# Kernel optimization log

Hardware: AMD Instinct MI355X
Metric: run time of the kernel (lower is better)

## Reference

```python
import jax, jax.numpy as jnp
import numpy as np

K_POS, K_NEG = 3, 2
MIN_D = 9  # min_dist=8 bumped to next odd, as in _nms_topk
BN_EPS = 1e-5


def _conv(x, w, pad):
    return jax.lax.conv_general_dilated(
        x, w, (1, 1), [(pad, pad), (pad, pad)],
        dimension_numbers=('NCHW', 'OIHW', 'NCHW'))


def _bn(x, g, b, m, v):
    scale = g * jax.lax.rsqrt(v + BN_EPS)  # inference-mode BN
    return x * scale[None, :, None, None] + (b - m * scale)[None, :, None, None]


def _head(x, w1, g1, b1, m1, v1, w2, g2, b2, m2, v2, w3, b3, out_hw):
    h = jax.nn.relu(_bn(_conv(x, w1, 1), g1, b1, m1, v1))
    h = jax.nn.relu(_bn(_conv(h, w2, 1), g2, b2, m2, v2))
    logits = _conv(h, w3, 0) + b3[None, :, None, None]
    B = logits.shape[0]
    # F.interpolate(mode='bilinear', align_corners=False) == half-pixel bilinear resize
    logits = jax.image.resize(logits, (B, 1, out_hw, out_hw), method='bilinear')
    return logits


def _sample_one(smap, key):
    # smap: [H, W] sigmoid heatmap for one sample
    H, W = smap.shape
    # --- positive points: NMS-style peak top-k ---
    local_max = jax.lax.reduce_window(
        smap, -jnp.inf, jax.lax.max, (MIN_D, MIN_D), (1, 1), 'SAME')
    is_peak = (smap == local_max) & (smap > 0.1)
    masked = jnp.where(is_peak, smap, -jnp.inf).reshape(-1)
    vals, idx = jax.lax.top_k(masked, K_POS)
    valid = jnp.isfinite(vals)  # slots corresponding to real peaks
    xs = jnp.where(valid, (idx % W).astype(jnp.float32), 0.0)
    ys = jnp.where(valid, (idx // W).astype(jnp.float32), 0.0)
    pos_lab = jnp.where(valid, 1, -1).astype(jnp.int32)
    # fallback: no peak at all -> single argmax point in slot 0
    amax = jnp.argmax(smap)
    any_peak = valid[0]
    xs = xs.at[0].set(jnp.where(any_peak, xs[0], (amax % W).astype(jnp.float32)))
    ys = ys.at[0].set(jnp.where(any_peak, ys[0], (amax // W).astype(jnp.float32)))
    pos_lab = pos_lab.at[0].set(1)  # slot 0 is always a positive point
    pos = jnp.stack([xs, ys], axis=1)  # [K_POS, 2] (x, y)
    # --- negative points: uniform sample from low-response region ---
    low = (smap < 0.3).reshape(-1)
    low_fb = (smap < smap.max()).reshape(-1)
    mask = jnp.where(jnp.any(low), low, low_fb)
    n = mask.sum()
    # stable argsort puts masked-in (True) flat indices first, in index order
    order = jnp.argsort(jnp.logical_not(mask))
    u = jax.random.uniform(key, (K_NEG,))
    ridx = jnp.minimum((u * jnp.maximum(n, 1).astype(jnp.float32)).astype(jnp.int32),
                       jnp.maximum(n - 1, 0))
    sel = order[ridx]
    neg = jnp.stack([sel % W, sel // W], axis=1).astype(jnp.float32)
    neg = jnp.where(n > 0, neg, jnp.zeros_like(neg))
    neg_lab = jnp.zeros((K_NEG,), jnp.int32)
    coords = jnp.concatenate([pos, neg], axis=0)      # [K_POS+K_NEG, 2]
    labels = jnp.concatenate([pos_lab, neg_lab], axis=0)
    return coords, labels


def setup_inputs() -> dict:
    key = jax.random.key(0)
    ks = jax.random.split(key, 4)
    B, C, h, w = 32, 256, 64, 64
    HID = 64
    x = jax.random.normal(ks[0], (B, C, h, w), jnp.float32)
    w1 = jax.random.normal(ks[1], (HID, C, 3, 3), jnp.float32) * 0.03  # kaiming-ish
    w2 = jax.random.normal(ks[2], (HID, HID, 3, 3), jnp.float32) * 0.06
    w3 = jax.random.normal(ks[3], (1, HID, 1, 1), jnp.float32) * 0.17
    b3 = jnp.full((1,), -2.0, jnp.float32)
    ones = jnp.ones((HID,), jnp.float32)
    zeros = jnp.zeros((HID,), jnp.float32)
    return {
        'encoder_features': x,
        'w1': w1, 'g1': ones, 'b1': zeros, 'm1': zeros, 'v1': ones,
        'w2': w2, 'g2': ones, 'b2': zeros, 'm2': zeros, 'v2': ones,
        'w3': w3, 'b3': b3,
        'output_size': 256,
    }


def reference(encoder_features, w1, g1, b1, m1, v1, w2, g2, b2, m2, v2, w3, b3, output_size):
    logits = _head(encoder_features, w1, g1, b1, m1, v1, w2, g2, b2, m2, v2, w3, b3, output_size)
    heatmap = jax.nn.sigmoid(logits)  # [B, 1, H, W]
    B = heatmap.shape[0]
    keys = jax.random.split(jax.random.key(42), B)
    coords, labels = jax.vmap(_sample_one)(heatmap[:, 0], keys)
    point_coords = coords[:, None].astype(jnp.float32)  # [B, 1, K, 2]
    point_labels = labels[:, None].astype(jnp.int32)    # [B, 1, K]
    return heatmap, point_coords, point_labels, logits
```

## Files before the change

### kernel.cpp

```cpp
#include <hip/hip_runtime.h>
#include <stdint.h>
#include <math.h>

#define NEG_INF (-__builtin_inff())
#define IDX_SENT 0x7fffffff

__device__ __forceinline__ void threefry2x32(uint32_t k0, uint32_t k1,
                                             uint32_t x0, uint32_t x1,
                                             uint32_t* o0, uint32_t* o1) {
  const uint32_t ks2 = k0 ^ k1 ^ 0x1BD11BDAu;
  uint32_t ks[3] = {k0, k1, ks2};
  const int rot[2][4] = {{13, 15, 26, 6}, {17, 29, 16, 24}};
  x0 += ks[0];
  x1 += ks[1];
#pragma unroll
  for (int i = 0; i < 5; ++i) {
#pragma unroll
    for (int j = 0; j < 4; ++j) {
      const int r = rot[i & 1][j];
      x0 += x1;
      x1 = (x1 << r) | (x1 >> (32 - r));
      x1 ^= x0;
    }
    x0 += ks[(i + 1) % 3];
    x1 += ks[(i + 2) % 3] + (uint32_t)(i + 1);
  }
  *o0 = x0;
  *o1 = x1;
}

__device__ __forceinline__ float bits_to_uniform(uint32_t bits) {
  return __uint_as_float((bits >> 9) | 0x3f800000u) - 1.0f;
}

__device__ __forceinline__ void top3_insert(float v, int idx, float tv[3], int ti[3]) {
  if ((v > tv[2]) || (v == tv[2] && idx < ti[2])) {
    tv[2] = v; ti[2] = idx;
    if ((tv[2] > tv[1]) || (tv[2] == tv[1] && ti[2] < ti[1])) {
      float fv = tv[1]; int fi = ti[1];
      tv[1] = tv[2]; ti[1] = ti[2];
      tv[2] = fv;     ti[2] = fi;
      if ((tv[1] > tv[0]) || (tv[1] == tv[0] && ti[1] < ti[0])) {
        fv = tv[0]; fi = ti[0];
        tv[0] = tv[1]; ti[0] = ti[1];
        tv[1] = fv;    ti[1] = fi;
      }
    }
  }
}

__global__ __launch_bounds__(256) void transpose_w4(
    const float* __restrict__ w, float* __restrict__ wt, int IC9) {
  const int idx = blockIdx.x * 256 + threadIdx.x;
  const int qrow = idx >> 6;
  const int oc = idx & 63;
  const float4 v = *(const float4*)&w[(size_t)oc * IC9 + qrow * 4];
  wt[(size_t)(qrow * 4 + 0) * 64 + oc] = v.x;
  wt[(size_t)(qrow * 4 + 1) * 64 + oc] = v.y;
  wt[(size_t)(qrow * 4 + 2) * 64 + oc] = v.z;
  wt[(size_t)(qrow * 4 + 3) * 64 + oc] = v.w;
}

template <int IC>
__global__ __launch_bounds__(256, 2) void conv3x3_bn_relu(
    const float* __restrict__ x, const float* __restrict__ wt,
    const float* __restrict__ g, const float* __restrict__ bb,
    const float* __restrict__ m, const float* __restrict__ vv,
    float* __restrict__ out) {
  __shared__ float xs[2][8][10][36];

  const int tid = threadIdx.x;
  const int blk = blockIdx.x;
  const int b = blk >> 4;
  const int tile = blk & 15;
  const int by = (tile >> 1) << 3;
  const int bx = (tile & 1) << 5;
  const int wv = __builtin_amdgcn_readfirstlane(tid >> 6);
  const int lane = tid & 63;
  const int r = lane & 7;
  const int lc = (lane >> 3) << 2;
  const int ocbase = wv << 4;

  const int sic = tid >> 5;
  const int sc = tid & 31;
  const int gx = bx + sc - 1;
  const bool cok = (gx >= 0) && (gx < 64);
  const bool xtra = (sc < 2);
  const int gx2 = bx + 31 + sc;
  const bool cok2 = xtra && (gx2 < 64);

  float acc[4][16];
#pragma unroll
  for (int p = 0; p < 4; ++p)
#pragma unroll
    for (int o = 0; o < 16; ++o) acc[p][o] = 0.0f;

  float pre[10];
  float preX[10];
  {
    const float* xp = x + ((size_t)b * IC + sic) * 4096;
#pragma unroll
    for (int rr = 0; rr < 10; ++rr) {
      const int gy = by + rr - 1;
      const bool rok = (gy >= 0) && (gy < 64);
      pre[rr] = 0.0f;
      preX[rr] = 0.0f;
      if (cok && rok) pre[rr] = xp[gy * 64 + gx];
      if (cok2 && rok) preX[rr] = xp[gy * 64 + gx2];
    }
#pragma unroll
    for (int rr = 0; rr < 10; ++rr) {
      xs[0][sic][rr][sc] = pre[rr];
      if (xtra) xs[0][sic][rr][32 + sc] = preX[rr];
    }
  }
  __syncthreads();

  int cur = 0;
  for (int icb = 0; icb < IC; icb += 8) {
    const bool has_next = (icb + 8) < IC;
    if (has_next) {
      const float* xp = x + ((size_t)b * IC + icb + 8 + sic) * 4096;
#pragma unroll
      for (int rr = 0; rr < 10; ++rr) {
        const int gy = by + rr - 1;
        const bool rok = (gy >= 0) && (gy < 64);
        pre[rr] = 0.0f;
        preX[rr] = 0.0f;
        if (cok && rok) pre[rr] = xp[gy * 64 + gx];
        if (cok2 && rok) preX[rr] = xp[gy * 64 + gx2];
      }
    }

    const float* wbase = wt + (size_t)icb * 9 * 64 + ocbase;
    for (int ic = 0; ic < 8; ++ic) {
#pragma unroll
      for (int ky = 0; ky < 3; ++ky) {
        float xv[6];
        *(float4*)&xv[0] = *(const float4*)&xs[cur][ic][r + ky][lc];
        *(float2*)&xv[4] = *(const float2*)&xs[cur][ic][r + ky][lc + 4];
#pragma unroll
        for (int kx = 0; kx < 3; ++kx) {
          const float4* wp4 = (const float4*)(wbase + (ic * 9 + ky * 3 + kx) * 64);
#pragma unroll
          for (int q = 0; q < 4; ++q) {
            const float4 w4 = wp4[q];
#pragma unroll
            for (int p = 0; p < 4; ++p) {
              acc[p][4 * q + 0] = fmaf(xv[kx + p], w4.x, acc[p][4 * q + 0]);
              acc[p][4 * q + 1] = fmaf(xv[kx + p], w4.y, acc[p][4 * q + 1]);
              acc[p][4 * q + 2] = fmaf(xv[kx + p], w4.z, acc[p][4 * q + 2]);
              acc[p][4 * q + 3] = fmaf(xv[kx + p], w4.w, acc[p][4 * q + 3]);
            }
          }
        }
      }
    }

    if (has_next) {
#pragma unroll
      for (int rr = 0; rr < 10; ++rr) {
        xs[cur ^ 1][sic][rr][sc] = pre[rr];
        if (xtra) xs[cur ^ 1][sic][rr][32 + sc] = preX[rr];
      }
    }
    __syncthreads();
    cur ^= 1;
  }

#pragma unroll
  for (int o = 0; o < 16; ++o) {
    const int oc = ocbase + o;
    const float sc2 = g[oc] * (1.0f / sqrtf(vv[oc] + 1e-5f));
    const float sh = bb[oc] - m[oc] * sc2;
    float4 v;
    v.x = fmaxf(fmaf(acc[0][o], sc2, sh), 0.0f);
    v.y = fmaxf(fmaf(acc[1][o], sc2, sh), 0.0f);
    v.z = fmaxf(fmaf(acc[2][o], sc2, sh), 0.0f);
    v.w = fmaxf(fmaf(acc[3][o], sc2, sh), 0.0f);
    *(float4*)&out[(((size_t)b * 64 + oc) * 64 + (by + r)) * 64 + bx + lc] = v;
  }
}

__global__ __launch_bounds__(256) void logits64_k(
    const float* __restrict__ h2, const float* __restrict__ w3,
    const float* __restrict__ b3, float* __restrict__ lg64) {
  const int blk = blockIdx.x;
  const int b = blk >> 4;
  const int p = ((blk & 15) << 8) + threadIdx.x;
  __shared__ float wvv[64];
  if (threadIdx.x < 64) wvv[threadIdx.x] = w3[threadIdx.x];
  __syncthreads();
  float s = b3[0];
  const float* hp = h2 + (size_t)b * 64 * 4096 + p;
  for (int oc = 0; oc < 64; ++oc)
    s = fmaf(hp[(size_t)oc * 4096], wvv[oc], s);
  lg64[b * 4096 + p] = s;
}

__global__ __launch_bounds__(256) void upsample_k(
    const float* __restrict__ lg64, float* __restrict__ logits,
    float* __restrict__ heat) {
  const int blk = blockIdx.x;
  const int b = blk >> 6;
  const int qq = ((blk & 63) << 10) + (threadIdx.x << 2);
  const float* lg = lg64 + b * 4096;
  const int oy = qq >> 8;
  const float sy = (float)oy * 0.25f - 0.375f;
  const float fy = floorf(sy);
  const int y0 = (int)fy;
  const float ty = sy - fy;
  const int y0c = y0 < 0 ? 0 : y0;
  const int y1c = (y0 + 1) > 63 ? 63 : (y0 + 1);
  const float* r0 = lg + y0c * 64;
  const float* r1 = lg + y1c * 64;
  float4 lo, he;
  float* lop = (float*)&lo;
  float* hep = (float*)&he;
#pragma unroll
  for (int j = 0; j < 4; ++j) {
    const int ox = (qq & 255) + j;
    const float sx = (float)ox * 0.25f - 0.375f;
    const float fx = floorf(sx);
    const int x0 = (int)fx;
    const float tx = sx - fx;
    const int x0c = x0 < 0 ? 0 : x0;
    const int x1c = (x0 + 1) > 63 ? 63 : (x0 + 1);
    const float v00 = r0[x0c], v01 = r0[x1c];
    const float v10 = r1[x0c], v11 = r1[x1c];
    const float vtop = v00 + (v01 - v00) * tx;
    const float vbot = v10 + (v11 - v10) * tx;
    const float val = vtop + (vbot - vtop) * ty;
    lop[j] = val;
    hep[j] = 1.0f / (1.0f + expf(-val));
  }
  const size_t o = (size_t)b * 65536 + qq;
  *(float4*)(logits + o) = lo;
  *(float4*)(heat + o) = he;
}

__global__ __launch_bounds__(256) void pos_stripe(
    const float* __restrict__ heat, float* __restrict__ cand) {
  const int b = blockIdx.x >> 4;
  const int stripe = blockIdx.x & 15;
  const int y0 = stripe << 4;
  const float* s = heat + (size_t)b * 65536;
  const int tid = threadIdx.x;
  __shared__ float sm[24][256];
  __shared__ float rm[24][256];
  __shared__ float rv[256 * 3];
  __shared__ int ri[256 * 3];
  __shared__ float mvv[256];
  __shared__ int mii[256];
  __shared__ float rv2[24];
  __shared__ int ri2[24];
  __shared__ float mv2[8];
  __shared__ int mi2[8];

  for (int l = tid; l < 24 * 256; l += 256) {
    const int rr = l >> 8, xx = l & 255;
    const int gy = y0 - 4 + rr;
    sm[rr][xx] = (gy >= 0 && gy < 256) ? s[gy * 256 + xx] : NEG_INF;
  }
  __syncthreads();
  for (int l = tid; l < 24 * 256; l += 256) {
    const int rr = l >> 8, xx = l & 255;
    const int lo = (xx - 4 < 0) ? 0 : xx - 4;
    const int hi = (xx + 4 > 255) ? 255 : xx + 4;
    float mx = NEG_INF;
    for (int x2 = lo; x2 <= hi; ++x2) mx = fmaxf(mx, sm[rr][x2]);
    rm[rr][xx] = mx;
  }
  __syncthreads();

  float tv[3] = {NEG_INF, NEG_INF, NEG_INF};
  int ti[3] = {IDX_SENT, IDX_SENT, IDX_SENT};
  float bmax = NEG_INF;
  int bidx = IDX_SENT;
  for (int l = tid; l < 16 * 256; l += 256) {
    const int ry = l >> 8, xx = l & 255;
    const int lr = ry + 4;
    const float v = sm[lr][xx];
    float lm = rm[lr - 4][xx];
#pragma unroll
    for (int d = -3; d <= 4; ++d) lm = fmaxf(lm, rm[lr + d][xx]);
    const int gidx = (y0 + ry) * 256 + xx;
    if (v > bmax) { bmax = v; bidx = gidx; }
    if (v == lm && v > 0.1f) top3_insert(v, gidx, tv, ti);
  }

  rv[tid * 3 + 0] = tv[0]; rv[tid * 3 + 1] = tv[1]; rv[tid * 3 + 2] = tv[2];
  ri[tid * 3 + 0] = ti[0]; ri[tid * 3 + 1] = ti[1]; ri[tid * 3 + 2] = ti[2];
  mvv[tid] = bmax; mii[tid] = bidx;
  __syncthreads();

  if (tid < 8) {
    float av[3] = {NEG_INF, NEG_INF, NEG_INF};
    int ai[3] = {IDX_SENT, IDX_SENT, IDX_SENT};
    float am = NEG_INF; int amI = IDX_SENT;
    for (int t = tid * 32; t < tid * 32 + 32; ++t) {
      for (int k = 0; k < 3; ++k) top3_insert(rv[t * 3 + k], ri[t * 3 + k], av, ai);
      if (mvv[t] > am || (mvv[t] == am && mii[t] < amI)) { am = mvv[t]; amI = mii[t]; }
    }
    rv2[tid * 3 + 0] = av[0]; rv2[tid * 3 + 1] = av[1]; rv2[tid * 3 + 2] = av[2];
    ri2[tid * 3 + 0] = ai[0]; ri2[tid * 3 + 1] = ai[1]; ri2[tid * 3 + 2] = ai[2];
    mv2[tid] = am; mi2[tid] = amI;
  }
  __syncthreads();

  if (tid == 0) {
    float fv[3] = {NEG_INF, NEG_INF, NEG_INF};
    int fi[3] = {IDX_SENT, IDX_SENT, IDX_SENT};
    for (int t = 0; t < 24; ++t) top3_insert(rv2[t], ri2[t], fv, fi);
    float gbv = NEG_INF; int gbi = IDX_SENT;
    for (int t = 0; t < 8; ++t)
      if (mv2[t] > gbv || (mv2[t] == gbv && mi2[t] < gbi)) { gbv = mv2[t]; gbi = mi2[t]; }
    float* c = cand + ((size_t)b * 16 + stripe) * 8;
    c[0] = fv[0]; c[1] = __int_as_float(fi[0]);
    c[2] = fv[1]; c[3] = __int_as_float(fi[1]);
    c[4] = fv[2]; c[5] = __int_as_float(fi[2]);
    c[6] = gbv;   c[7] = __int_as_float(gbi);
  }
}

__global__ void pos_final(const float* __restrict__ cand,
                          float* __restrict__ coords, float* __restrict__ labels) {
  const int b = blockIdx.x;
  if (threadIdx.x != 0) return;
  float fv[3] = {NEG_INF, NEG_INF, NEG_INF};
  int fi[3] = {IDX_SENT, IDX_SENT, IDX_SENT};
  float gbv = NEG_INF; int gbi = IDX_SENT;
  for (int st = 0; st < 16; ++st) {
    const float* c = cand + ((size_t)b * 16 + st) * 8;
    for (int k = 0; k < 3; ++k)
      top3_insert(c[2 * k], __float_as_int(c[2 * k + 1]), fv, fi);
    const float mv = c[6]; const int mi = __float_as_int(c[7]);
    if (mv > gbv || (mv == gbv && mi < gbi)) { gbv = mv; gbi = mi; }
  }
  float* co = coords + (size_t)b * 10;
  float* la = labels + (size_t)b * 5;
  const bool any_peak = (fi[0] != IDX_SENT);
  const int i0 = any_peak ? fi[0] : gbi;
  co[0] = (float)(i0 & 255);
  co[1] = (float)(i0 >> 8);
  la[0] = 1.0f;
  for (int k = 1; k < 3; ++k) {
    const bool valid = (fi[k] != IDX_SENT);
    co[k * 2 + 0] = valid ? (float)(fi[k] & 255) : 0.0f;
    co[k * 2 + 1] = valid ? (float)(fi[k] >> 8) : 0.0f;
    la[k] = valid ? 1.0f : -1.0f;
  }
}

__global__ __launch_bounds__(256) void neg_count(
    const float* __restrict__ heat, float* __restrict__ ncnt,
    float* __restrict__ pmax) {
  const int blk = blockIdx.x;
  const int b = blk >> 2;
  const int part = blk & 3;
  const int tid = threadIdx.x;
  const int chunk = (part << 8) + tid;
  const float4* s = (const float4*)(heat + (size_t)b * 65536 + chunk * 64);
  int c = 0;
  float mx = NEG_INF;
  for (int i = 0; i < 16; ++i) {
    const float4 v = s[i];
    c += (v.x < 0.3f) + (v.y < 0.3f) + (v.z < 0.3f) + (v.w < 0.3f);
    mx = fmaxf(mx, fmaxf(fmaxf(v.x, v.y), fmaxf(v.z, v.w)));
  }
  ncnt[b * 1024 + chunk] = (float)c;
  __shared__ float mxs[256];
  mxs[tid] = mx;
  __syncthreads();
  if (tid == 0) {
    float gmx = NEG_INF;
    for (int t = 0; t < 256; ++t) gmx = fmaxf(gmx, mxs[t]);
    pmax[blk] = gmx;
  }
}

__global__ __launch_bounds__(256) void neg_select(
    const float* __restrict__ heat, const float* __restrict__ ncnt,
    const float* __restrict__ pmax, float* __restrict__ coords,
    float* __restrict__ labels) {
  const int b = blockIdx.x;
  const int tid = threadIdx.x;
  const float* s = heat + (size_t)b * 65536;
  __shared__ float cnt[1024];
  __shared__ float c256[256];
  __shared__ int pfx[257];
  __shared__ float thr_s;
  __shared__ int fb_s;
  __shared__ int n_s;
  __shared__ int ridx_s[2];

  for (int l = tid; l < 1024; l += 256) cnt[l] = ncnt[b * 1024 + l];
  __syncthreads();
  c256[tid] = cnt[4 * tid] + cnt[4 * tid + 1] + cnt[4 * tid + 2] + cnt[4 * tid + 3];
  __syncthreads();
  if (tid == 0) {
    int tot = 0;
    for (int t = 0; t < 256; ++t) tot += (int)c256[t];
    const float gm = fmaxf(fmaxf(pmax[b * 4], pmax[b * 4 + 1]),
                           fmaxf(pmax[b * 4 + 2], pmax[b * 4 + 3]));
    fb_s = (tot > 0) ? 0 : 1;
    thr_s = (tot > 0) ? 0.3f : gm;
  }
  __syncthreads();
  if (fb_s) {
    const float t2 = thr_s;
    const int base = tid * 256;
    int c = 0;
    for (int i = 0; i < 256; ++i) c += (s[base + i] < t2) ? 1 : 0;
    c256[tid] = (float)c;
    __syncthreads();
  }
  if (tid == 0) {
    int run = 0;
    for (int t = 0; t < 256; ++t) { pfx[t] = run; run += (int)c256[t]; }
    pfx[256] = run;
    const int n = run;
    n_s = n;
    uint32_t k0, k1, a0, a1;
    threefry2x32(0u, 42u, 0u, (uint32_t)b, &k0, &k1);
    threefry2x32(k0, k1, 0u, 0u, &a0, &a1);
    const uint32_t bits0 = a0 ^ a1;
    threefry2x32(k0, k1, 0u, 1u, &a0, &a1);
    const uint32_t bits1 = a0 ^ a1;
    const float u0 = bits_to_uniform(bits0);
    const float u1 = bits_to_uniform(bits1);
    const float nf = (float)(n > 1 ? n : 1);
    int r0 = (int)(u0 * nf);
    int r1 = (int)(u1 * nf);
    const int rmax = (n - 1 > 0) ? n - 1 : 0;
    ridx_s[0] = r0 < rmax ? r0 : rmax;
    ridx_s[1] = r1 < rmax ? r1 : rmax;
    labels[(size_t)b * 5 + 3] = 0.0f;
    labels[(size_t)b * 5 + 4] = 0.0f;
    if (n == 0) {
      coords[(size_t)b * 10 + 6] = 0.0f; coords[(size_t)b * 10 + 7] = 0.0f;
      coords[(size_t)b * 10 + 8] = 0.0f; coords[(size_t)b * 10 + 9] = 0.0f;
    }
  }
  __syncthreads();
  const int n = n_s;
  if (n > 0) {
    const float t2 = thr_s;
    const int p0 = pfx[tid], p1 = pfx[tid + 1];
    const int base = tid * 256;
    for (int j = 0; j < 2; ++j) {
      const int r = ridx_s[j];
      if (r >= p0 && r < p1) {
        int need = r - p0;
        int sel = -1;
        for (int i = 0; i < 256; ++i) {
          if (s[base + i] < t2) {
            if (need == 0) { sel = base + i; break; }
            --need;
          }
        }
        coords[(size_t)b * 10 + 6 + j * 2 + 0] = (float)(sel & 255);
        coords[(size_t)b * 10 + 6 + j * 2 + 1] = (float)(sel >> 8);
      }
    }
  }
}

extern "C" void kernel_launch(void* const* d_in, const int* in_sizes, int n_in,
                              void* d_out, int out_size, void* d_ws, size_t ws_size,
                              hipStream_t stream) {
  (void)in_sizes; (void)n_in; (void)out_size; (void)ws_size;
  const float* x  = (const float*)d_in[0];
  const float* w1 = (const float*)d_in[1];
  const float* g1 = (const float*)d_in[2];
  const float* b1 = (const float*)d_in[3];
  const float* m1 = (const float*)d_in[4];
  const float* v1 = (const float*)d_in[5];
  const float* w2 = (const float*)d_in[6];
  const float* g2 = (const float*)d_in[7];
  const float* b2 = (const float*)d_in[8];
  const float* m2 = (const float*)d_in[9];
  const float* v2 = (const float*)d_in[10];
  const float* w3 = (const float*)d_in[11];
  const float* b3 = (const float*)d_in[12];

  float* out = (float*)d_out;
  float* heat = out;
  float* coords = out + (size_t)32 * 65536;
  float* labels = coords + 320;
  float* logits = labels + 160;

  float* w1t = logits;
  float* w2t = logits + 147456;

  float* h1 = (float*)d_ws;
  float* h2 = h1 + (size_t)32 * 64 * 64 * 64;
  float* lg64 = h1;
  float* cand = h1 + 131072;
  float* ncnt = h1 + 135168;
  float* pmax = h1 + 167936;

  transpose_w4<<<144, 256, 0, stream>>>(w1, w1t, 2304);
  transpose_w4<<<36, 256, 0, stream>>>(w2, w2t, 576);
  conv3x3_bn_relu<256><<<512, 256, 0, stream>>>(x, w1t, g1, b1, m1, v1, h1);
  conv3x3_bn_relu<64><<<512, 256, 0, stream>>>(h1, w2t, g2, b2, m2, v2, h2);
  logits64_k<<<512, 256, 0, stream>>>(h2, w3, b3, lg64);
  upsample_k<<<2048, 256, 0, stream>>>(lg64, logits, heat);
  pos_stripe<<<512, 256, 0, stream>>>(heat, cand);
  pos_final<<<32, 64, 0, stream>>>(cand, coords, labels);
  neg_count<<<128, 256, 0, stream>>>(heat, ncnt, pmax);
  neg_select<<<32, 256, 0, stream>>>(heat, ncnt, pmax, coords, labels);
}
```

Before: 789.4 us.

## Double conv block to 512 threads with 8 output channels per wave

```diff
diff --git a/kernel.cpp b/kernel.cpp
--- a/kernel.cpp
+++ b/kernel.cpp
@@ -62,7 +62,7 @@
 }
 
 template <int IC>
-__global__ __launch_bounds__(256, 2) void conv3x3_bn_relu(
+__global__ __launch_bounds__(512, 4) void conv3x3_bn_relu(
     const float* __restrict__ x, const float* __restrict__ wt,
     const float* __restrict__ g, const float* __restrict__ bb,
     const float* __restrict__ m, const float* __restrict__ vv,
@@ -79,40 +79,31 @@
   const int lane = tid & 63;
   const int r = lane & 7;
   const int lc = (lane >> 3) << 2;
-  const int ocbase = wv << 4;
-
-  const int sic = tid >> 5;
-  const int sc = tid & 31;
+  const int ocbase = wv << 3;
+
+  const int sic = wv;
+  const int sc = lane;
   const int gx = bx + sc - 1;
-  const bool cok = (gx >= 0) && (gx < 64);
-  const bool xtra = (sc < 2);
-  const int gx2 = bx + 31 + sc;
-  const bool cok2 = xtra && (gx2 < 64);
-
-  float acc[4][16];
+  const bool cok = (sc < 34) && (gx >= 0) && (gx < 64);
+
+  float acc[4][8];
 #pragma unroll
   for (int p = 0; p < 4; ++p)
 #pragma unroll
-    for (int o = 0; o < 16; ++o) acc[p][o] = 0.0f;
+    for (int o = 0; o < 8; ++o) acc[p][o] = 0.0f;
 
   float pre[10];
-  float preX[10];
   {
     const float* xp = x + ((size_t)b * IC + sic) * 4096;
 #pragma unroll
     for (int rr = 0; rr < 10; ++rr) {
       const int gy = by + rr - 1;
-      const bool rok = (gy >= 0) && (gy < 64);
       pre[rr] = 0.0f;
-      preX[rr] = 0.0f;
-      if (cok && rok) pre[rr] = xp[gy * 64 + gx];
-      if (cok2 && rok) preX[rr] = xp[gy * 64 + gx2];
-    }
-#pragma unroll
-    for (int rr = 0; rr < 10; ++rr) {
-      xs[0][sic][rr][sc] = pre[rr];
-      if (xtra) xs[0][sic][rr][32 + sc] = preX[rr];
-    }
+      if (cok && gy >= 0 && gy < 64) pre[rr] = xp[gy * 64 + gx];
+    }
+#pragma unroll
+    for (int rr = 0; rr < 10; ++rr)
+      if (sc < 34) xs[0][sic][rr][sc] = pre[rr];
   }
   __syncthreads();
 
@@ -124,11 +115,8 @@
 #pragma unroll
       for (int rr = 0; rr < 10; ++rr) {
         const int gy = by + rr - 1;
-        const bool rok = (gy >= 0) && (gy < 64);
         pre[rr] = 0.0f;
-        preX[rr] = 0.0f;
-        if (cok && rok) pre[rr] = xp[gy * 64 + gx];
-        if (cok2 && rok) preX[rr] = xp[gy * 64 + gx2];
+        if (cok && gy >= 0 && gy < 64) pre[rr] = xp[gy * 64 + gx];
       }
     }
 
@@ -143,7 +131,7 @@
         for (int kx = 0; kx < 3; ++kx) {
           const float4* wp4 = (const float4*)(wbase + (ic * 9 + ky * 3 + kx) * 64);
 #pragma unroll
-          for (int q = 0; q < 4; ++q) {
+          for (int q = 0; q < 2; ++q) {
             const float4 w4 = wp4[q];
 #pragma unroll
             for (int p = 0; p < 4; ++p) {
@@ -159,17 +147,15 @@
 
     if (has_next) {
 #pragma unroll
-      for (int rr = 0; rr < 10; ++rr) {
-        xs[cur ^ 1][sic][rr][sc] = pre[rr];
-        if (xtra) xs[cur ^ 1][sic][rr][32 + sc] = preX[rr];
-      }
+      for (int rr = 0; rr < 10; ++rr)
+        if (sc < 34) xs[cur ^ 1][sic][rr][sc] = pre[rr];
     }
     __syncthreads();
     cur ^= 1;
   }
 
 #pragma unroll
-  for (int o = 0; o < 16; ++o) {
+  for (int o = 0; o < 8; ++o) {
     const int oc = ocbase + o;
     const float sc2 = g[oc] * (1.0f / sqrtf(vv[oc] + 1e-5f));
     const float sh = bb[oc] - m[oc] * sc2;
@@ -502,8 +488,8 @@
 
   transpose_w4<<<144, 256, 0, stream>>>(w1, w1t, 2304);
   transpose_w4<<<36, 256, 0, stream>>>(w2, w2t, 576);
-  conv3x3_bn_relu<256><<<512, 256, 0, stream>>>(x, w1t, g1, b1, m1, v1, h1);
-  conv3x3_bn_relu<64><<<512, 256, 0, stream>>>(h1, w2t, g2, b2, m2, v2, h2);
+  conv3x3_bn_relu<256><<<512, 512, 0, stream>>>(x, w1t, g1, b1, m1, v1, h1);
+  conv3x3_bn_relu<64><<<512, 512, 0, stream>>>(h1, w2t, g2, b2, m2, v2, h2);
   logits64_k<<<512, 256, 0, stream>>>(h2, w3, b3, lg64);
   upsample_k<<<2048, 256, 0, stream>>>(lg64, logits, heat);
   pos_stripe<<<512, 256, 0, stream>>>(heat, cand);
```

After: 782.0 us. Within noise of the previous version (-0.9%).
